# Kernel tuning notes

Measured on AMD Instinct MI355X. Metric: run time of the kernel, lower is better.

## Reference

```python
import jax, jax.numpy as jnp
import numpy as np

INF = 1.0e6  # sentinel distance for rows/cols with no background pixel


def _edt(mask):
    """Exact 2D Euclidean distance transform.

    For each pixel of mask [B,C,H,W], returns the Euclidean distance to the
    nearest pixel where mask == 0 (scipy.ndimage.distance_transform_edt
    semantics: nonzero = foreground, zero = background/feature).
    Uses the separable 2-pass algorithm: 1D distance along H, then an exact
    min over parabolas along W (done as a vectorized scan over column index).
    """
    B, C, H, W = mask.shape
    is_fg = mask != 0  # [B,C,H,W]

    # ---- pass 1: 1D distance along axis H to nearest zero in same column ----
    fg_h = jnp.moveaxis(is_fg, 2, 0)  # [H,B,C,W]

    def run_step(d, fg_row):  # d: [B,C,W]
        d = jnp.where(fg_row, d + 1.0, 0.0)
        return d, d

    init = jnp.full((B, C, W), INF, jnp.float32)
    _, d_fwd = jax.lax.scan(run_step, init, fg_h)
    _, d_bwd = jax.lax.scan(run_step, init, fg_h, reverse=True)
    g = jnp.minimum(jnp.minimum(d_fwd, d_bwd), INF)  # [H,B,C,W]
    f = jnp.moveaxis(g * g, 0, 2)  # [B,C,H,W] squared vertical distance

    # ---- pass 2: D[...,j] = min_k (j-k)^2 + f[...,k]  (exact 2D sq. EDT) ----
    js = jnp.arange(W, dtype=jnp.float32)  # [W]
    f_k = jnp.moveaxis(f, 3, 0)  # [W,B,C,H]

    def min_step(D, xs):
        k, fk = xs  # scalar, [B,C,H]
        cand = (js - k) ** 2 + fk[..., None]  # [B,C,H,W]
        return jnp.minimum(D, cand), None

    D0 = jnp.full((B, C, H, W), INF * INF, jnp.float32)
    D, _ = jax.lax.scan(min_step, D0, (js, f_k))
    return jnp.sqrt(D)


def setup_inputs() -> dict:
    key = jax.random.key(0)
    k1, k2 = jax.random.split(key)
    B, C, H, W = 16, 1, 512, 512
    output = jax.random.normal(k1, (B, C, H, W), dtype=jnp.float32)
    target = jax.random.randint(k2, (B, C, H, W), 0, 2, dtype=jnp.int32)
    return {"output": output, "target": target}


def reference(output, target):
    prob = jax.nn.sigmoid(output)  # [B,C,H,W]
    tgt = target.astype(jnp.float32)
    # signed distance: distance inside foreground minus distance inside background
    dist = _edt(1.0 - tgt) - _edt(tgt)  # [B,C,H,W]
    return jnp.mean(prob * dist)
```

## Files before the change

### kernel.cpp

```cpp
#include <hip/hip_runtime.h>
#include <math.h>

#define HDIM 512
#define WDIM 512
#define SEG 16
#define SROWS 32
#define VCOLS 32
#define VTHREADS 512
#define ROWS_PB 4
#define HTHREADS 256
#define PAD 16
#define LROW (WDIM + 2 * PAD)
#define INF_I (1 << 20)
#define ENC_SENT 127


__global__ __launch_bounds__(VTHREADS) void vert_pass10(const int* __restrict__ tgt,
                                                        signed char* __restrict__ sdist) {
    __shared__ int s_fs1[SEG][VCOLS], s_ls1[SEG][VCOLS];
    __shared__ int s_fs0[SEG][VCOLS], s_ls0[SEG][VCOLS];
    __shared__ int s_c1f[SEG][VCOLS], s_c1b[SEG][VCOLS];
    __shared__ int s_c0f[SEG][VCOLS], s_c0b[SEG][VCOLS];

    int tid = threadIdx.x;
    int w = tid & (VCOLS - 1);
    int seg = tid >> 5;
    int bW = WDIM / VCOLS;
    int b = blockIdx.x / bW;
    int wbase = (blockIdx.x % bW) * VCOLS;
    size_t colbase = (size_t)b * HDIM * WDIM + wbase + w;
    const int* col = tgt + colbase + (size_t)(seg * SROWS) * WDIM;

    unsigned R1 = 0u;
    #pragma unroll 8
    for (int h = 0; h < SROWS; ++h) {
        int tv = col[(size_t)h * WDIM];
        R1 |= ((unsigned)(tv != 0)) << h;
    }
    unsigned R0 = ~R1;

    s_fs1[seg][w] = R1 ? __builtin_ctz(R1) : SROWS;
    s_ls1[seg][w] = R1 ? 31 - __builtin_clz(R1) : -1;
    s_fs0[seg][w] = R0 ? __builtin_ctz(R0) : SROWS;
    s_ls0[seg][w] = R0 ? 31 - __builtin_clz(R0) : -1;
    __syncthreads();

    if (tid < 128) {
        int cw = tid & (VCOLS - 1);
        int md = tid >> 5;
        int c = INF_I;
        if (md == 0) {
            for (int s = 0; s < SEG; ++s) {
                s_c1f[s][cw] = c;
                int ls = s_ls1[s][cw];
                c = (ls >= 0) ? (SROWS - 1 - ls) : c + SROWS;
            }
        } else if (md == 1) {
            for (int s = SEG - 1; s >= 0; --s) {
                s_c1b[s][cw] = c;
                int fs = s_fs1[s][cw];
                c = (fs < SROWS) ? fs : c + SROWS;
            }
        } else if (md == 2) {
            for (int s = 0; s < SEG; ++s) {
                s_c0f[s][cw] = c;
                int ls = s_ls0[s][cw];
                c = (ls >= 0) ? (SROWS - 1 - ls) : c + SROWS;
            }
        } else {
            for (int s = SEG - 1; s >= 0; --s) {
                s_c0b[s][cw] = c;
                int fs = s_fs0[s][cw];
                c = (fs < SROWS) ? fs : c + SROWS;
            }
        }
    }
    __syncthreads();

    int c1f = s_c1f[seg][w], c1b = s_c1b[seg][w];
    int c0f = s_c0f[seg][w], c0b = s_c0b[seg][w];

    signed char* os = sdist + colbase + (size_t)(seg * SROWS) * WDIM;

    unsigned mle = 0u;
    for (int h = 0; h < SROWS; ++h) {
        mle = (mle << 1) | 1u;
        unsigned a1 = R1 & mle;
        int d1f = a1 ? (h - (31 - __builtin_clz(a1))) : c1f + h + 1;
        unsigned b1 = R1 >> h;
        int d1b = b1 ? __builtin_ctz(b1) : c1b + (SROWS - h);
        int g1 = min(d1f, d1b);
        unsigned a0 = R0 & mle;
        int d0f = a0 ? (h - (31 - __builtin_clz(a0))) : c0f + h + 1;
        unsigned b0 = R0 >> h;
        int d0b = b0 ? __builtin_ctz(b0) : c0b + (SROWS - h);
        int g0 = min(d0f, d0b);

        signed char sval = ((R1 >> h) & 1u) ? (signed char)(-min(g0, ENC_SENT))
                                            : (signed char)min(g1, ENC_SENT);
        os[(size_t)h * WDIM] = sval;
    }
}

__global__ __launch_bounds__(HTHREADS) void horiz_pass10(const int* __restrict__ sdist4,
                                                         const float* __restrict__ outp,
                                                         double* __restrict__ partial) {
    __shared__ float sf1[ROWS_PB * LROW];
    __shared__ float sf0[ROWS_PB * LROW];
    __shared__ double swave[4];

    int tid = threadIdx.x;
    size_t base = (size_t)blockIdx.x * (ROWS_PB * WDIM);

    if (tid < ROWS_PB * 2 * PAD) {
        int r = tid / (2 * PAD);
        int c = tid % (2 * PAD);
        int off = r * LROW + (c < PAD ? c : WDIM + c);
        sf1[off] = 3.0e12f;
        sf0[off] = 3.0e12f;
    }

    const int* sp = sdist4 + base / 4;
    for (int i = tid; i < (ROWS_PB * WDIM) / 4; i += HTHREADS) {
        int p = sp[i];
        int j = i * 4;
        int row = j >> 9;
        int lbase = row * LROW + PAD + (j & (WDIM - 1));
        float4 q1, q0;
        float* q1f = (float*)&q1;
        float* q0f = (float*)&q0;
        #pragma unroll
        for (int k = 0; k < 4; ++k) {
            int sv = (p << (24 - 8 * k)) >> 24;
            int neg = sv < 0;
            int e = neg ? -sv : sv;
            float g = (e >= ENC_SENT) ? 1.0e6f : (float)e;
            float f = g * g;
            q1f[k] = neg ? 0.0f : f;
            q0f[k] = neg ? f : 0.0f;
        }
        *(float4*)(sf1 + lbase) = q1;
        *(float4*)(sf0 + lbase) = q0;
    }
    __syncthreads();

    double local = 0.0;

    #pragma unroll
    for (int g = 0; g < 2; ++g) {
        int idx0 = (g * HTHREADS + tid) * 4;
        int row = idx0 >> 9;
        int j0 = idx0 & (WDIM - 1);
        int wb = row * LROW + PAD + j0;
        float4 xq = *(const float4*)(outp + base + idx0);

        float w1[16], w0[16];
        *(float4*)(w1 + 0)  = *(const float4*)(sf1 + wb - 8);
        *(float4*)(w1 + 4)  = *(const float4*)(sf1 + wb - 4);
        *(float4*)(w1 + 8)  = *(const float4*)(sf1 + wb + 0);
        *(float4*)(w1 + 12) = *(const float4*)(sf1 + wb + 4);
        *(float4*)(w0 + 0)  = *(const float4*)(sf0 + wb - 8);
        *(float4*)(w0 + 4)  = *(const float4*)(sf0 + wb - 4);
        *(float4*)(w0 + 8)  = *(const float4*)(sf0 + wb + 0);
        *(float4*)(w0 + 12) = *(const float4*)(sf0 + wb + 4);

        float best[4];
        bool cls[4];
        #pragma unroll
        for (int q = 0; q < 4; ++q) {
            bool c0 = w1[8 + q] > 0.0f;
            cls[q] = c0;
            float b = c0 ? w1[8 + q] : w0[8 + q];
            #pragma unroll
            for (int rad = 1; rad <= 4; ++rad) {
                float rr = (float)(rad * rad);
                float cl = c0 ? w1[8 + q - rad] : w0[8 + q - rad];
                float cr = c0 ? w1[8 + q + rad] : w0[8 + q + rad];
                b = fminf(b, fminf(rr + cl, rr + cr));
            }
            best[q] = b;
        }

        float qmax = fmaxf(fmaxf(best[0], best[1]), fmaxf(best[2], best[3]));
        if (qmax > 25.0f) {
            float e1[4], e0[4];
            *(float4*)e1 = *(const float4*)(sf1 + wb + 8);
            *(float4*)e0 = *(const float4*)(sf0 + wb + 8);
            #pragma unroll
            for (int q = 0; q < 4; ++q) {
                bool c0 = cls[q];
                float b = best[q];
                #pragma unroll
                for (int rad = 5; rad <= 8; ++rad) {
                    float rr = (float)(rad * rad);
                    int li = 8 + q - rad;
                    int ri = 8 + q + rad;
                    float cl = c0 ? w1[li] : w0[li];
                    float cr = (ri < 16) ? (c0 ? w1[ri] : w0[ri])
                                         : (c0 ? e1[ri - 16] : e0[ri - 16]);
                    b = fminf(b, fminf(rr + cl, rr + cr));
                }
                best[q] = b;
            }
            #pragma unroll
            for (int q = 0; q < 4; ++q) {
                if (best[q] > 81.0f) {
                    int j = j0 + q;
                    const float* env = (cls[q] ? sf1 : sf0) + row * LROW + PAD;
                    float b = best[q];
                    float rr = 81.0f;
                    for (int rad = 9; rad < WDIM; ++rad) {
                        if (rr >= b) break;
                        int kl = j - rad; kl = kl < 0 ? 0 : kl;
                        int kr = j + rad; kr = kr > WDIM - 1 ? WDIM - 1 : kr;
                        b = fminf(b, fminf(rr + env[kl], rr + env[kr]));
                        rr += 2.0f * (float)rad + 1.0f;
                    }
                    best[q] = b;
                }
            }
        }

        const float* xs = (const float*)&xq;
        #pragma unroll
        for (int q = 0; q < 4; ++q) {
            float sd = sqrtf(best[q]);
            float dist = cls[q] ? sd : -sd;
            float prob = 1.0f / (1.0f + expf(-xs[q]));
            local += (double)(prob * dist);
        }
    }

    double v = local;
    #pragma unroll
    for (int off = 32; off > 0; off >>= 1) v += __shfl_down(v, off, 64);
    int wid = tid >> 6, lane = tid & 63;
    if (lane == 0) swave[wid] = v;
    __syncthreads();
    if (tid == 0) partial[blockIdx.x] = swave[0] + swave[1] + swave[2] + swave[3];
}

__global__ __launch_bounds__(256) void finalize10(const double* __restrict__ partial,
                                                  float* __restrict__ out,
                                                  int npart, double invN) {
    __shared__ double swave[4];
    int tid = threadIdx.x;
    double local = 0.0;
    for (int i = tid; i < npart; i += 256) local += partial[i];
    #pragma unroll
    for (int off = 32; off > 0; off >>= 1) local += __shfl_down(local, off, 64);
    int wid = tid >> 6, lane = tid & 63;
    if (lane == 0) swave[wid] = local;
    __syncthreads();
    if (tid == 0) out[0] = (float)((swave[0] + swave[1] + swave[2] + swave[3]) * invN);
}

extern "C" void kernel_launch(void* const* d_in, const int* in_sizes, int n_in,
                              void* d_out, int out_size, void* d_ws, size_t ws_size,
                              hipStream_t stream) {
    const float* outp = (const float*)d_in[0];
    const int* tgt = (const int*)d_in[1];
    int N = in_sizes[0];
    int B = N / (HDIM * WDIM);

    int npart = (B * HDIM) / ROWS_PB;

    double* partial = (double*)((char*)d_ws + 256);
    signed char* sdist = (signed char*)((char*)d_ws + 32768);

    vert_pass10<<<B * (WDIM / VCOLS), VTHREADS, 0, stream>>>(tgt, sdist);
    horiz_pass10<<<npart, HTHREADS, 0, stream>>>((const int*)sdist, outp, partial);
    finalize10<<<1, 256, 0, stream>>>(partial, (float*)d_out, npart, 1.0 / (double)N);
}
```

Baseline: 28.36 us.

## Prefetch logits early, use fast math intrinsics and float accumulation in horizontal pass

Issues the global loads of the logits and packed distances at kernel start so they overlap with shared-memory staging. It simplifies decoding by squaring the signed byte directly, hoists the radius add out of the min, and swaps sqrt, exp and divide for fast intrinsics. Per-thread and per-wave accumulation moves from double to float. This cuts FP64 work and instruction count, at the cost of slightly lower precision in the sum and the sigmoid.

```diff
diff --git a/kernel.cpp b/kernel.cpp
--- a/kernel.cpp
+++ b/kernel.cpp
@@ -15,7 +15,7 @@
 #define ENC_SENT 127
 
 
-__global__ __launch_bounds__(VTHREADS) void vert_pass10(const int* __restrict__ tgt,
+__global__ __launch_bounds__(VTHREADS) void vert_pass12(const int* __restrict__ tgt,
                                                         signed char* __restrict__ sdist) {
     __shared__ int s_fs1[SEG][VCOLS], s_ls1[SEG][VCOLS];
     __shared__ int s_fs0[SEG][VCOLS], s_ls0[SEG][VCOLS];
@@ -102,7 +102,7 @@
     }
 }
 
-__global__ __launch_bounds__(HTHREADS) void horiz_pass10(const int* __restrict__ sdist4,
+__global__ __launch_bounds__(HTHREADS) void horiz_pass12(const int* __restrict__ sdist4,
                                                          const float* __restrict__ outp,
                                                          double* __restrict__ partial) {
     __shared__ float sf1[ROWS_PB * LROW];
@@ -111,6 +111,9 @@
 
     int tid = threadIdx.x;
     size_t base = (size_t)blockIdx.x * (ROWS_PB * WDIM);
+
+    float4 xq0 = *(const float4*)(outp + base + tid * 4);
+    float4 xq1 = *(const float4*)(outp + base + (HTHREADS + tid) * 4);
 
     if (tid < ROWS_PB * 2 * PAD) {
         int r = tid / (2 * PAD);
@@ -121,9 +124,12 @@
     }
 
     const int* sp = sdist4 + base / 4;
-    for (int i = tid; i < (ROWS_PB * WDIM) / 4; i += HTHREADS) {
-        int p = sp[i];
-        int j = i * 4;
+    int pk0 = sp[tid];
+    int pk1 = sp[HTHREADS + tid];
+    #pragma unroll
+    for (int g = 0; g < 2; ++g) {
+        int p = g ? pk1 : pk0;
+        int j = (g * HTHREADS + tid) * 4;
         int row = j >> 9;
         int lbase = row * LROW + PAD + (j & (WDIM - 1));
         float4 q1, q0;
@@ -132,10 +138,10 @@
         #pragma unroll
         for (int k = 0; k < 4; ++k) {
             int sv = (p << (24 - 8 * k)) >> 24;
-            int neg = sv < 0;
-            int e = neg ? -sv : sv;
-            float g = (e >= ENC_SENT) ? 1.0e6f : (float)e;
-            float f = g * g;
+            int e2 = sv * sv;
+            float f = (float)e2;
+            f = (e2 == ENC_SENT * ENC_SENT) ? 1.0e12f : f;
+            bool neg = sv < 0;
             q1f[k] = neg ? 0.0f : f;
             q0f[k] = neg ? f : 0.0f;
         }
@@ -144,7 +150,7 @@
     }
     __syncthreads();
 
-    double local = 0.0;
+    float local = 0.0f;
 
     #pragma unroll
     for (int g = 0; g < 2; ++g) {
@@ -152,7 +158,7 @@
         int row = idx0 >> 9;
         int j0 = idx0 & (WDIM - 1);
         int wb = row * LROW + PAD + j0;
-        float4 xq = *(const float4*)(outp + base + idx0);
+        float4 xq = g ? xq1 : xq0;
 
         float w1[16], w0[16];
         *(float4*)(w1 + 0)  = *(const float4*)(sf1 + wb - 8);
@@ -176,7 +182,7 @@
                 float rr = (float)(rad * rad);
                 float cl = c0 ? w1[8 + q - rad] : w0[8 + q - rad];
                 float cr = c0 ? w1[8 + q + rad] : w0[8 + q + rad];
-                b = fminf(b, fminf(rr + cl, rr + cr));
+                b = fminf(b, rr + fminf(cl, cr));
             }
             best[q] = b;
         }
@@ -198,7 +204,7 @@
                     float cl = c0 ? w1[li] : w0[li];
                     float cr = (ri < 16) ? (c0 ? w1[ri] : w0[ri])
                                          : (c0 ? e1[ri - 16] : e0[ri - 16]);
-                    b = fminf(b, fminf(rr + cl, rr + cr));
+                    b = fminf(b, rr + fminf(cl, cr));
                 }
                 best[q] = b;
             }
@@ -224,23 +230,23 @@
         const float* xs = (const float*)&xq;
         #pragma unroll
         for (int q = 0; q < 4; ++q) {
-            float sd = sqrtf(best[q]);
+            float sd = __builtin_amdgcn_sqrtf(best[q]);
             float dist = cls[q] ? sd : -sd;
-            float prob = 1.0f / (1.0f + expf(-xs[q]));
-            local += (double)(prob * dist);
-        }
-    }
-
-    double v = local;
+            float prob = __fdividef(1.0f, 1.0f + __expf(-xs[q]));
+            local += prob * dist;
+        }
+    }
+
+    float v = local;
     #pragma unroll
     for (int off = 32; off > 0; off >>= 1) v += __shfl_down(v, off, 64);
     int wid = tid >> 6, lane = tid & 63;
-    if (lane == 0) swave[wid] = v;
+    if (lane == 0) swave[wid] = (double)v;
     __syncthreads();
     if (tid == 0) partial[blockIdx.x] = swave[0] + swave[1] + swave[2] + swave[3];
 }
 
-__global__ __launch_bounds__(256) void finalize10(const double* __restrict__ partial,
+__global__ __launch_bounds__(256) void finalize12(const double* __restrict__ partial,
                                                   float* __restrict__ out,
                                                   int npart, double invN) {
     __shared__ double swave[4];
@@ -268,7 +274,7 @@
     double* partial = (double*)((char*)d_ws + 256);
     signed char* sdist = (signed char*)((char*)d_ws + 32768);
 
-    vert_pass10<<<B * (WDIM / VCOLS), VTHREADS, 0, stream>>>(tgt, sdist);
-    horiz_pass10<<<npart, HTHREADS, 0, stream>>>((const int*)sdist, outp, partial);
-    finalize10<<<1, 256, 0, stream>>>(partial, (float*)d_out, npart, 1.0 / (double)N);
-}
+    vert_pass12<<<B * (WDIM / VCOLS), VTHREADS, 0, stream>>>(tgt, sdist);
+    horiz_pass12<<<npart, HTHREADS, 0, stream>>>((const int*)sdist, outp, partial);
+    finalize12<<<1, 256, 0, stream>>>(partial, (float*)d_out, npart, 1.0 / (double)N);
+}
```

Result: no change. 28.52 us (+0.6%).
